# Performance work log

Measured on AMD Instinct MI355X. Metric: run time of the kernel, lower is better.

## Reference

```python
import jax, jax.numpy as jnp
import numpy as np

N_NODES = 10000
N_EDGES = 640000
IN_DIM = 128
OUT_DIM = 128


def setup_inputs() -> dict:
    key = jax.random.key(0)
    k1, k2, k3, k4, k5 = jax.random.split(key, 5)
    h = jax.random.normal(k1, (N_NODES, IN_DIM), dtype=jnp.float32)
    src = jax.random.randint(k2, (N_EDGES,), 0, N_NODES, dtype=jnp.int32)
    dst = jax.random.randint(k3, (N_EDGES,), 0, N_NODES, dtype=jnp.int32)
    # nn.Linear default init: U(-1/sqrt(fan_in), 1/sqrt(fan_in)); scale normals similarly
    W_fc = jax.random.normal(k4, (OUT_DIM, IN_DIM), dtype=jnp.float32) / np.sqrt(IN_DIM)
    W_attn = jax.random.normal(k5, (1, 2 * OUT_DIM), dtype=jnp.float32) / np.sqrt(2 * OUT_DIM)
    return {"h": h, "src": src, "dst": dst, "W_fc": W_fc, "W_attn": W_attn}


def reference(h, src, dst, W_fc, W_attn):
    n = h.shape[0]
    # z = fc(h)
    z = h @ W_fc.T                                   # [N, out]
    # edge attention: attn_fc(cat([z_src, z_dst])) == z_src @ a_s + z_dst @ a_d
    a_src = W_attn[0, :OUT_DIM]                      # [out]
    a_dst = W_attn[0, OUT_DIM:]                      # [out]
    e = z @ a_src                                    # [N] per-node src contribution
    f = z @ a_dst                                    # [N] per-node dst contribution
    score = e[src] + f[dst]                          # [E] edge logits
    # segment softmax over incoming edges of each dst node
    m = jax.ops.segment_max(score, dst, num_segments=n)   # [N]
    m = jnp.where(jnp.isfinite(m), m, 0.0)                # guard empty segments
    ex = jnp.exp(score - m[dst])                           # [E]
    den = jax.ops.segment_sum(ex, dst, num_segments=n)     # [N]
    alpha = ex / jnp.where(den > 0, den, 1.0)[dst]          # [E]
    # weighted scatter-sum of source z into dst
    msg = alpha[:, None] * z[src]                           # [E, out]
    h_out = jax.ops.segment_sum(msg, dst, num_segments=n)  # [N, out]
    return h_out
```

## Files before the change

kernel.cpp:

```cpp
#include <hip/hip_runtime.h>

#define NN 10000
#define NE 640000
#define DIM 128
#define HNB 64
#define HEPB 10000
#define FCN 64
#define FCB ((NN + FCN - 1) / FCN)
#define PAD 128

static __device__ __forceinline__ unsigned short f2bf(float f) {
    unsigned u = __float_as_uint(f);
    unsigned r = (u + 0x7FFFu + ((u >> 16) & 1u)) >> 16;
    return (unsigned short)r;
}
static __device__ __forceinline__ float bfhi(unsigned u) { return __uint_as_float(u & 0xFFFF0000u); }
static __device__ __forceinline__ float bflo(unsigned u) { return __uint_as_float(u << 16); }

__global__ __launch_bounds__(512) void histT_kernel(
    const int* __restrict__ dst, int* __restrict__ bh,
    const float* __restrict__ W, float* __restrict__ Wt)
{
    __shared__ int lh[NN];
    const int b = blockIdx.x, t = threadIdx.x;
    for (int v = t; v < NN; v += 512) lh[v] = 0;
    if (t < 256) {
        int idx = b * 256 + t;
        Wt[(idx & 127) * DIM + (idx >> 7)] = W[idx];
    }
    __syncthreads();
    const int4* d4 = (const int4*)(dst + b * HEPB);
    for (int i = t; i < HEPB / 4; i += 512) {
        int4 d = d4[i];
        atomicAdd(&lh[d.x], 1); atomicAdd(&lh[d.y], 1);
        atomicAdd(&lh[d.z], 1); atomicAdd(&lh[d.w], 1);
    }
    __syncthreads();
    for (int v = t; v < NN; v += 512) bh[(size_t)b * NN + v] = lh[v];
}

__global__ __launch_bounds__(512) void colscan_kernel(
    int* __restrict__ bh, int* __restrict__ cnt)
{
    const int lane = threadIdx.x & 63, w = threadIdx.x >> 6;
    const int v = blockIdx.x * 8 + w;
    int c = bh[(size_t)lane * NN + v];
    int x = c;
    #pragma unroll
    for (int o = 1; o <= 32; o <<= 1) {
        int y = __shfl_up(x, o, 64);
        if (lane >= o) x += y;
    }
    bh[(size_t)lane * NN + v] = x - c;
    if (lane == 63) cnt[v] = x;
}

__global__ __launch_bounds__(512, 2) void scatfc_kernel(
    const int* __restrict__ src, const int* __restrict__ dst,
    const int* __restrict__ base, int* __restrict__ esrc,
    const float* __restrict__ h, const float* __restrict__ Wt,
    const float* __restrict__ Wa, unsigned short* __restrict__ zb,
    float* __restrict__ e)
{
    __shared__ int smem[10240];
    const int bid = blockIdx.x, t = threadIdx.x;

    if (bid < HNB) {
        int* lcur = smem;
        for (int v = t; v < NN; v += 512) lcur[v] = 0;
        __syncthreads();
        const int4* d4 = (const int4*)(dst + bid * HEPB);
        const int4* s4 = (const int4*)(src + bid * HEPB);
        const int* brow = base + (size_t)bid * NN;
        for (int i = t; i < HEPB / 4; i += 512) {
            int4 d = d4[i]; int4 s = s4[i];
            int r;
            r = brow[d.x] + atomicAdd(&lcur[d.x], 1); if (r < PAD) esrc[(d.x << 7) + r] = s.x;
            r = brow[d.y] + atomicAdd(&lcur[d.y], 1); if (r < PAD) esrc[(d.y << 7) + r] = s.y;
            r = brow[d.z] + atomicAdd(&lcur[d.z], 1); if (r < PAD) esrc[(d.z << 7) + r] = s.z;
            r = brow[d.w] + atomicAdd(&lcur[d.w], 1); if (r < PAD) esrc[(d.w << 7) + r] = s.w;
        }
    } else {
        float* hs = (float*)smem;
        const int jl = t & 31, jq = jl * 4;
        const int ng = t >> 5;
        const int i0 = (bid - HNB) * FCN;

        const float4* h4 = (const float4*)h;
        float4* hs4 = (float4*)hs;
        for (int u = t; u < FCN * 32; u += 512) {
            int gi = i0 + (u >> 5);
            hs4[u] = (gi < NN) ? h4[(size_t)gi * 32 + (u & 31)]
                               : make_float4(0.f, 0.f, 0.f, 0.f);
        }
        __syncthreads();

        float acc[4][4] = {};
        for (int k = 0; k < DIM; k += 4) {
            float4 wv[4];
            #pragma unroll
            for (int kk = 0; kk < 4; ++kk)
                wv[kk] = *(const float4*)&Wt[(k + kk) * DIM + jq];
            const float* wf = (const float*)wv;
            #pragma unroll
            for (int m = 0; m < 4; ++m) {
                float4 hv = *(const float4*)&hs[(4 * ng + m) * DIM + k];
                float hvf[4] = {hv.x, hv.y, hv.z, hv.w};
                #pragma unroll
                for (int kk = 0; kk < 4; ++kk)
                    #pragma unroll
                    for (int jm = 0; jm < 4; ++jm)
                        acc[m][jm] += hvf[kk] * wf[kk * 4 + jm];
            }
        }

        const float a0 = Wa[jq], a1 = Wa[jq + 1], a2 = Wa[jq + 2], a3 = Wa[jq + 3];
        #pragma unroll
        for (int m = 0; m < 4; ++m) {
            int gi = i0 + 4 * ng + m;
            float ep = acc[m][0] * a0 + acc[m][1] * a1 + acc[m][2] * a2 + acc[m][3] * a3;
            #pragma unroll
            for (int o = 16; o > 0; o >>= 1) ep += __shfl_xor(ep, o, 64);
            if (gi < NN) {
                ushort4 zo;
                zo.x = f2bf(acc[m][0]); zo.y = f2bf(acc[m][1]);
                zo.z = f2bf(acc[m][2]); zo.w = f2bf(acc[m][3]);
                *(ushort4*)&zb[(size_t)gi * DIM + jq] = zo;
                if (jl == 0) e[gi] = ep;
            }
        }
    }
}

__global__ __launch_bounds__(256) void agg_kernel(
    const int* __restrict__ cnt, const int* __restrict__ esrc,
    const float* __restrict__ e, const unsigned* __restrict__ zb32,
    float* __restrict__ out)
{
    __shared__ int   es[4][PAD];
    __shared__ float ew[4][PAD];
    const int w = threadIdx.x >> 6, lane = threadIdx.x & 63;
    const int v = blockIdx.x * 4 + w;
    if (v >= NN) return;
    int* esw = es[w];
    float* eww = ew[w];
    const int beg = v << 7;
    int deg = cnt[v];
    if (deg > PAD) deg = PAD;

    float lm = -3.4e38f;
    #pragma unroll
    for (int i = lane; i < PAD; i += 64) {
        if (i < deg) {
            int s = esrc[beg + i];
            float ev = e[s];
            esw[i] = s; eww[i] = ev;
            lm = fmaxf(lm, ev);
        }
    }
    #pragma unroll
    for (int o = 32; o > 0; o >>= 1) lm = fmaxf(lm, __shfl_xor(lm, o, 64));

    float ls = 0.f;
    #pragma unroll
    for (int i = lane; i < PAD; i += 64) {
        if (i < deg) {
            float p = __expf(eww[i] - lm);
            eww[i] = p; ls += p;
        }
    }
    #pragma unroll
    for (int o = 32; o > 0; o >>= 1) ls += __shfl_xor(ls, o, 64);
    const float inv = (ls > 0.f) ? (1.f / ls) : 0.f;

    const uint2* zb2 = (const uint2*)zb32;
    const int half = lane >> 5, hl = lane & 31;
    float a0 = 0.f, a1 = 0.f, a2 = 0.f, a3 = 0.f;
    int i = half;
    for (; i + 6 < deg; i += 8) {
        int   s0 = esw[i],  s1 = esw[i + 2],  s2 = esw[i + 4],  s3 = esw[i + 6];
        float w0 = eww[i],  w1 = eww[i + 2],  w2 = eww[i + 4],  w3 = eww[i + 6];
        uint2 u0 = zb2[(size_t)s0 * 32 + hl];
        uint2 u1 = zb2[(size_t)s1 * 32 + hl];
        uint2 u2 = zb2[(size_t)s2 * 32 + hl];
        uint2 u3 = zb2[(size_t)s3 * 32 + hl];
        a0 += w0 * bflo(u0.x); a1 += w0 * bfhi(u0.x);
        a2 += w0 * bflo(u0.y); a3 += w0 * bfhi(u0.y);
        a0 += w1 * bflo(u1.x); a1 += w1 * bfhi(u1.x);
        a2 += w1 * bflo(u1.y); a3 += w1 * bfhi(u1.y);
        a0 += w2 * bflo(u2.x); a1 += w2 * bfhi(u2.x);
        a2 += w2 * bflo(u2.y); a3 += w2 * bfhi(u2.y);
        a0 += w3 * bflo(u3.x); a1 += w3 * bfhi(u3.x);
        a2 += w3 * bflo(u3.y); a3 += w3 * bfhi(u3.y);
    }
    for (; i < deg; i += 2) {
        int s = esw[i]; float p = eww[i];
        uint2 u = zb2[(size_t)s * 32 + hl];
        a0 += p * bflo(u.x); a1 += p * bfhi(u.x);
        a2 += p * bflo(u.y); a3 += p * bfhi(u.y);
    }
    a0 += __shfl_xor(a0, 32, 64);
    a1 += __shfl_xor(a1, 32, 64);
    a2 += __shfl_xor(a2, 32, 64);
    a3 += __shfl_xor(a3, 32, 64);
    if (half == 0) {
        float4 r;
        r.x = a0 * inv; r.y = a1 * inv; r.z = a2 * inv; r.w = a3 * inv;
        *(float4*)&out[(size_t)v * DIM + 4 * hl] = r;
    }
}

extern "C" void kernel_launch(void* const* d_in, const int* in_sizes, int n_in,
                              void* d_out, int out_size, void* d_ws, size_t ws_size,
                              hipStream_t stream)
{
    const float* h     = (const float*)d_in[0];
    const int*   src   = (const int*)d_in[1];
    const int*   dst   = (const int*)d_in[2];
    const float* Wfc   = (const float*)d_in[3];
    const float* Wattn = (const float*)d_in[4];
    float* out = (float*)d_out;

    unsigned short* zb   = (unsigned short*)d_ws;
    float*          e    = (float*)(zb + (size_t)NN * DIM + 16);
    int*            cnt  = (int*)(e + 10016);
    float*          Wt   = (float*)(cnt + 10016);
    int*            bh   = (int*)(Wt + 16384);
    int*            esrc = bh + (size_t)HNB * NN;

    histT_kernel<<<HNB, 512, 0, stream>>>(dst, bh, Wfc, Wt);
    colscan_kernel<<<NN / 8, 512, 0, stream>>>(bh, cnt);
    scatfc_kernel<<<HNB + FCB, 512, 0, stream>>>(src, dst, bh, esrc,
                                                 h, Wt, Wattn, zb, e);
    agg_kernel<<<(NN + 3) / 4, 256, 0, stream>>>(cnt, esrc, e, (const unsigned*)zb, out);
}
```

Before: 55.80 us.

## Fuse column prefix scan into scatter kernel, removing colscan launch

Removes the separate colscan kernel. Each scatter block now computes its own exclusive prefix by summing the histogram rows of all earlier blocks straight into shared memory, and the last block writes the total counts. This saves one kernel launch and the read-write pass over the histogram, but block b now reads b rows, giving quadratic redundant reads (about 2016 rows of 40KB in total) that are concentrated in the high-index blocks.

```diff
diff --git a/kernel.cpp b/kernel.cpp
--- a/kernel.cpp
+++ b/kernel.cpp
@@ -39,25 +39,9 @@
     for (int v = t; v < NN; v += 512) bh[(size_t)b * NN + v] = lh[v];
 }
 
-__global__ __launch_bounds__(512) void colscan_kernel(
-    int* __restrict__ bh, int* __restrict__ cnt)
-{
-    const int lane = threadIdx.x & 63, w = threadIdx.x >> 6;
-    const int v = blockIdx.x * 8 + w;
-    int c = bh[(size_t)lane * NN + v];
-    int x = c;
-    #pragma unroll
-    for (int o = 1; o <= 32; o <<= 1) {
-        int y = __shfl_up(x, o, 64);
-        if (lane >= o) x += y;
-    }
-    bh[(size_t)lane * NN + v] = x - c;
-    if (lane == 63) cnt[v] = x;
-}
-
 __global__ __launch_bounds__(512, 2) void scatfc_kernel(
     const int* __restrict__ src, const int* __restrict__ dst,
-    const int* __restrict__ base, int* __restrict__ esrc,
+    const int* __restrict__ bh, int* __restrict__ cnt, int* __restrict__ esrc,
     const float* __restrict__ h, const float* __restrict__ Wt,
     const float* __restrict__ Wa, unsigned short* __restrict__ zb,
     float* __restrict__ e)
@@ -67,18 +51,44 @@
 
     if (bid < HNB) {
         int* lcur = smem;
-        for (int v = t; v < NN; v += 512) lcur[v] = 0;
+        const int4* bh4 = (const int4*)bh;
+        int4 acc[5];
+        #pragma unroll
+        for (int j = 0; j < 5; ++j) acc[j] = make_int4(0, 0, 0, 0);
+        for (int b = 0; b < bid; ++b) {
+            const int4* row = bh4 + (size_t)b * 2500;
+            #pragma unroll
+            for (int j = 0; j < 5; ++j) {
+                int c4 = t + j * 512;
+                if (c4 < 2500) {
+                    int4 x = row[c4];
+                    acc[j].x += x.x; acc[j].y += x.y;
+                    acc[j].z += x.z; acc[j].w += x.w;
+                }
+            }
+        }
+        int4* lcur4 = (int4*)lcur;
+        #pragma unroll
+        for (int j = 0; j < 5; ++j) {
+            int c4 = t + j * 512;
+            if (c4 < 2500) lcur4[c4] = acc[j];
+        }
         __syncthreads();
+
         const int4* d4 = (const int4*)(dst + bid * HEPB);
         const int4* s4 = (const int4*)(src + bid * HEPB);
-        const int* brow = base + (size_t)bid * NN;
         for (int i = t; i < HEPB / 4; i += 512) {
             int4 d = d4[i]; int4 s = s4[i];
             int r;
-            r = brow[d.x] + atomicAdd(&lcur[d.x], 1); if (r < PAD) esrc[(d.x << 7) + r] = s.x;
-            r = brow[d.y] + atomicAdd(&lcur[d.y], 1); if (r < PAD) esrc[(d.y << 7) + r] = s.y;
-            r = brow[d.z] + atomicAdd(&lcur[d.z], 1); if (r < PAD) esrc[(d.z << 7) + r] = s.z;
-            r = brow[d.w] + atomicAdd(&lcur[d.w], 1); if (r < PAD) esrc[(d.w << 7) + r] = s.w;
+            r = atomicAdd(&lcur[d.x], 1); if (r < PAD) esrc[(d.x << 7) + r] = s.x;
+            r = atomicAdd(&lcur[d.y], 1); if (r < PAD) esrc[(d.y << 7) + r] = s.y;
+            r = atomicAdd(&lcur[d.z], 1); if (r < PAD) esrc[(d.z << 7) + r] = s.z;
+            r = atomicAdd(&lcur[d.w], 1); if (r < PAD) esrc[(d.w << 7) + r] = s.w;
+        }
+
+        if (bid == HNB - 1) {
+            __syncthreads();
+            for (int v = t; v < NN; v += 512) cnt[v] = lcur[v];
         }
     } else {
         float* hs = (float*)smem;
@@ -229,8 +239,7 @@
     int*            esrc = bh + (size_t)HNB * NN;
 
     histT_kernel<<<HNB, 512, 0, stream>>>(dst, bh, Wfc, Wt);
-    colscan_kernel<<<NN / 8, 512, 0, stream>>>(bh, cnt);
-    scatfc_kernel<<<HNB + FCB, 512, 0, stream>>>(src, dst, bh, esrc,
+    scatfc_kernel<<<HNB + FCB, 512, 0, stream>>>(src, dst, bh, cnt, esrc,
                                                  h, Wt, Wattn, zb, e);
     agg_kernel<<<(NN + 3) / 4, 256, 0, stream>>>(cnt, esrc, e, (const unsigned*)zb, out);
 }
```

Measured after the change: 81.01 us. 45.2% more time.

## Replace histogram/scan CSR build with per-block bucketed slots and in-agg compaction

Applied to the files above, without the earlier changes.

Removes the separate histogram and column-scan kernels. Each of 32 scatter blocks now writes source indices into its own fixed 16-slot bucket per destination node, and the aggregation kernel prefix-scans the 32 bucket counts per node and compacts the slots into shared memory. The FC matmul now reads W directly instead of a transposed copy, which removes the transpose step. This cuts two kernel launches and a pass over dst. In exchange, esrc grows to 512 slots per node, and a node that gets more than 16 edges from one block would have edges silently dropped.

```diff
diff --git a/kernel.cpp b/kernel.cpp
--- a/kernel.cpp
+++ b/kernel.cpp
@@ -3,11 +3,13 @@
 #define NN 10000
 #define NE 640000
 #define DIM 128
-#define HNB 64
-#define HEPB 10000
+#define SB 32
+#define SEPB (NE / SB)
+#define CAP 16
+#define SLOTS (SB * CAP)
 #define FCN 64
 #define FCB ((NN + FCN - 1) / FCN)
-#define PAD 128
+#define DCAP 128
 
 static __device__ __forceinline__ unsigned short f2bf(float f) {
     unsigned u = __float_as_uint(f);
@@ -17,74 +19,38 @@
 static __device__ __forceinline__ float bfhi(unsigned u) { return __uint_as_float(u & 0xFFFF0000u); }
 static __device__ __forceinline__ float bflo(unsigned u) { return __uint_as_float(u << 16); }
 
-__global__ __launch_bounds__(512) void histT_kernel(
-    const int* __restrict__ dst, int* __restrict__ bh,
-    const float* __restrict__ W, float* __restrict__ Wt)
-{
-    __shared__ int lh[NN];
-    const int b = blockIdx.x, t = threadIdx.x;
-    for (int v = t; v < NN; v += 512) lh[v] = 0;
-    if (t < 256) {
-        int idx = b * 256 + t;
-        Wt[(idx & 127) * DIM + (idx >> 7)] = W[idx];
-    }
-    __syncthreads();
-    const int4* d4 = (const int4*)(dst + b * HEPB);
-    for (int i = t; i < HEPB / 4; i += 512) {
-        int4 d = d4[i];
-        atomicAdd(&lh[d.x], 1); atomicAdd(&lh[d.y], 1);
-        atomicAdd(&lh[d.z], 1); atomicAdd(&lh[d.w], 1);
-    }
-    __syncthreads();
-    for (int v = t; v < NN; v += 512) bh[(size_t)b * NN + v] = lh[v];
-}
-
-__global__ __launch_bounds__(512) void colscan_kernel(
-    int* __restrict__ bh, int* __restrict__ cnt)
-{
-    const int lane = threadIdx.x & 63, w = threadIdx.x >> 6;
-    const int v = blockIdx.x * 8 + w;
-    int c = bh[(size_t)lane * NN + v];
-    int x = c;
-    #pragma unroll
-    for (int o = 1; o <= 32; o <<= 1) {
-        int y = __shfl_up(x, o, 64);
-        if (lane >= o) x += y;
-    }
-    bh[(size_t)lane * NN + v] = x - c;
-    if (lane == 63) cnt[v] = x;
-}
-
 __global__ __launch_bounds__(512, 2) void scatfc_kernel(
     const int* __restrict__ src, const int* __restrict__ dst,
-    const int* __restrict__ base, int* __restrict__ esrc,
-    const float* __restrict__ h, const float* __restrict__ Wt,
+    int* __restrict__ bhcnt, int* __restrict__ esrc,
+    const float* __restrict__ h, const float* __restrict__ W,
     const float* __restrict__ Wa, unsigned short* __restrict__ zb,
     float* __restrict__ e)
 {
     __shared__ int smem[10240];
     const int bid = blockIdx.x, t = threadIdx.x;
 
-    if (bid < HNB) {
+    if (bid < SB) {
         int* lcur = smem;
         for (int v = t; v < NN; v += 512) lcur[v] = 0;
         __syncthreads();
-        const int4* d4 = (const int4*)(dst + bid * HEPB);
-        const int4* s4 = (const int4*)(src + bid * HEPB);
-        const int* brow = base + (size_t)bid * NN;
-        for (int i = t; i < HEPB / 4; i += 512) {
+        const int4* d4 = (const int4*)(dst + bid * SEPB);
+        const int4* s4 = (const int4*)(src + bid * SEPB);
+        const int boff = bid * CAP;
+        for (int i = t; i < SEPB / 4; i += 512) {
             int4 d = d4[i]; int4 s = s4[i];
             int r;
-            r = brow[d.x] + atomicAdd(&lcur[d.x], 1); if (r < PAD) esrc[(d.x << 7) + r] = s.x;
-            r = brow[d.y] + atomicAdd(&lcur[d.y], 1); if (r < PAD) esrc[(d.y << 7) + r] = s.y;
-            r = brow[d.z] + atomicAdd(&lcur[d.z], 1); if (r < PAD) esrc[(d.z << 7) + r] = s.z;
-            r = brow[d.w] + atomicAdd(&lcur[d.w], 1); if (r < PAD) esrc[(d.w << 7) + r] = s.w;
-        }
+            r = atomicAdd(&lcur[d.x], 1); if (r < CAP) esrc[(d.x << 9) + boff + r] = s.x;
+            r = atomicAdd(&lcur[d.y], 1); if (r < CAP) esrc[(d.y << 9) + boff + r] = s.y;
+            r = atomicAdd(&lcur[d.z], 1); if (r < CAP) esrc[(d.z << 9) + boff + r] = s.z;
+            r = atomicAdd(&lcur[d.w], 1); if (r < CAP) esrc[(d.w << 9) + boff + r] = s.w;
+        }
+        __syncthreads();
+        for (int v = t; v < NN; v += 512) bhcnt[(size_t)bid * NN + v] = lcur[v];
     } else {
         float* hs = (float*)smem;
         const int jl = t & 31, jq = jl * 4;
         const int ng = t >> 5;
-        const int i0 = (bid - HNB) * FCN;
+        const int i0 = (bid - SB) * FCN;
 
         const float4* h4 = (const float4*)h;
         float4* hs4 = (float4*)hs;
@@ -95,22 +61,20 @@
         }
         __syncthreads();
 
+        const float4* W4 = (const float4*)W;
         float acc[4][4] = {};
-        for (int k = 0; k < DIM; k += 4) {
-            float4 wv[4];
+        for (int kq = 0; kq < 32; ++kq) {
+            float4 wrow[4];
             #pragma unroll
-            for (int kk = 0; kk < 4; ++kk)
-                wv[kk] = *(const float4*)&Wt[(k + kk) * DIM + jq];
-            const float* wf = (const float*)wv;
+            for (int jm = 0; jm < 4; ++jm)
+                wrow[jm] = W4[(size_t)(jq + jm) * 32 + kq];
             #pragma unroll
             for (int m = 0; m < 4; ++m) {
-                float4 hv = *(const float4*)&hs[(4 * ng + m) * DIM + k];
-                float hvf[4] = {hv.x, hv.y, hv.z, hv.w};
+                float4 hv = *(const float4*)&hs[(4 * ng + m) * DIM + 4 * kq];
                 #pragma unroll
-                for (int kk = 0; kk < 4; ++kk)
-                    #pragma unroll
-                    for (int jm = 0; jm < 4; ++jm)
-                        acc[m][jm] += hvf[kk] * wf[kk * 4 + jm];
+                for (int jm = 0; jm < 4; ++jm)
+                    acc[m][jm] += hv.x * wrow[jm].x + hv.y * wrow[jm].y
+                                + hv.z * wrow[jm].z + hv.w * wrow[jm].w;
             }
         }
 
@@ -133,41 +97,61 @@
 }
 
 __global__ __launch_bounds__(256) void agg_kernel(
-    const int* __restrict__ cnt, const int* __restrict__ esrc,
+    const int* __restrict__ bhcnt, const int* __restrict__ esrc,
     const float* __restrict__ e, const unsigned* __restrict__ zb32,
     float* __restrict__ out)
 {
-    __shared__ int   es[4][PAD];
-    __shared__ float ew[4][PAD];
+    __shared__ int   es[4][DCAP];
+    __shared__ float ew[4][DCAP];
     const int w = threadIdx.x >> 6, lane = threadIdx.x & 63;
     const int v = blockIdx.x * 4 + w;
-    if (v >= NN) return;
     int* esw = es[w];
     float* eww = ew[w];
-    const int beg = v << 7;
-    int deg = cnt[v];
-    if (deg > PAD) deg = PAD;
+
+    int c = 0;
+    if (lane < SB) {
+        c = bhcnt[(size_t)lane * NN + v];
+        if (c > CAP) c = CAP;
+    }
+    int x = c;
+    #pragma unroll
+    for (int o = 1; o <= 16; o <<= 1) {
+        int y = __shfl_up(x, o, 64);
+        if (lane >= o) x += y;
+    }
+    int deg = __shfl(x, SB - 1, 64);
+    if (deg > DCAP) deg = DCAP;
+    const int excl = x - c;
+    const int myb   = lane >> 1;
+    const int mycnt = __shfl(c, myb, 64);
+    const int mybase = __shfl(excl, myb, 64);
+
+    const int4* sp = (const int4*)&esrc[(size_t)v * SLOTS + lane * 8];
+    int4 q0 = sp[0], q1 = sp[1];
+    int sv[8] = {q0.x, q0.y, q0.z, q0.w, q1.x, q1.y, q1.z, q1.w};
+    const int rbase = (lane & 1) * 8;
+    #pragma unroll
+    for (int jj = 0; jj < 8; ++jj) {
+        int r = rbase + jj;
+        if (r < mycnt) {
+            int tgt = mybase + r;
+            if (tgt < DCAP) {
+                int s = sv[jj];
+                esw[tgt] = s;
+                eww[tgt] = e[s];
+            }
+        }
+    }
 
     float lm = -3.4e38f;
-    #pragma unroll
-    for (int i = lane; i < PAD; i += 64) {
-        if (i < deg) {
-            int s = esrc[beg + i];
-            float ev = e[s];
-            esw[i] = s; eww[i] = ev;
-            lm = fmaxf(lm, ev);
-        }
-    }
+    for (int i = lane; i < deg; i += 64) lm = fmaxf(lm, eww[i]);
     #pragma unroll
     for (int o = 32; o > 0; o >>= 1) lm = fmaxf(lm, __shfl_xor(lm, o, 64));
 
     float ls = 0.f;
-    #pragma unroll
-    for (int i = lane; i < PAD; i += 64) {
-        if (i < deg) {
-            float p = __expf(eww[i] - lm);
-            eww[i] = p; ls += p;
-        }
+    for (int i = lane; i < deg; i += 64) {
+        float p = __expf(eww[i] - lm);
+        eww[i] = p; ls += p;
     }
     #pragma unroll
     for (int o = 32; o > 0; o >>= 1) ls += __shfl_xor(ls, o, 64);
@@ -221,16 +205,12 @@
     const float* Wattn = (const float*)d_in[4];
     float* out = (float*)d_out;
 
-    unsigned short* zb   = (unsigned short*)d_ws;
-    float*          e    = (float*)(zb + (size_t)NN * DIM + 16);
-    int*            cnt  = (int*)(e + 10016);
-    float*          Wt   = (float*)(cnt + 10016);
-    int*            bh   = (int*)(Wt + 16384);
-    int*            esrc = bh + (size_t)HNB * NN;
-
-    histT_kernel<<<HNB, 512, 0, stream>>>(dst, bh, Wfc, Wt);
-    colscan_kernel<<<NN / 8, 512, 0, stream>>>(bh, cnt);
-    scatfc_kernel<<<HNB + FCB, 512, 0, stream>>>(src, dst, bh, esrc,
-                                                 h, Wt, Wattn, zb, e);
-    agg_kernel<<<(NN + 3) / 4, 256, 0, stream>>>(cnt, esrc, e, (const unsigned*)zb, out);
-}
+    unsigned short* zb    = (unsigned short*)d_ws;
+    float*          e     = (float*)(zb + (size_t)NN * DIM);
+    int*            bhcnt = (int*)(e + 10016);
+    int*            esrc  = bhcnt + (size_t)SB * NN;
+
+    scatfc_kernel<<<SB + FCB, 512, 0, stream>>>(src, dst, bhcnt, esrc,
+                                                h, Wfc, Wattn, zb, e);
+    agg_kernel<<<NN / 4, 256, 0, stream>>>(bhcnt, esrc, e, (const unsigned*)zb, out);
+}
```

Result: slower. 61.03 us (+9.4%).
